# Kernel tuning notes

Hardware: AMD Instinct MI355X
Metric: run time of the kernel (lower is better)

## Reference

```python
import jax, jax.numpy as jnp
import numpy as np

DIM = 384
H = 65536
P = 3
CORR = 2 * 49 * P * P  # 882


def _lin(x, W, b):
    # x: [H, Cin], W: [Cout, Cin], b: [Cout] -> [H, Cout] (1x1 conv == linear over channels)
    return x @ W.T + b


def setup_inputs() -> dict:
    key = jax.random.key(0)
    ks = jax.random.split(key, 20)
    f32 = jnp.float32

    def rn(k, shape, s=0.02):
        return jax.random.normal(k, shape, f32) * s

    return {
        "net": jax.random.normal(ks[0], (1, DIM, H, 1), f32),
        "inp": jax.random.normal(ks[1], (1, DIM, H, 1), f32),
        "corr": jax.random.normal(ks[2], (1, CORR, H, 1), f32),
        "ii": jax.random.normal(ks[3], (1, 1, H, 1), f32),
        "jj": jax.random.normal(ks[4], (1, 1, H, 1), f32),
        "kk": jax.random.normal(ks[5], (1, 1, H, 1), f32),
        # keep_conv: Conv2d(1,1,1,bias=False) with weight zeroed (frozen)
        "kw": jnp.zeros((), f32),
        # corr_conv: Linear(882->384), ReLU, Linear(384->384), ReLU, Linear(384->384)
        "cc_w1": rn(ks[6], (DIM, CORR)), "cc_b1": jnp.zeros((DIM,), f32),
        "cc_w2": rn(ks[7], (DIM, DIM)), "cc_b2": jnp.zeros((DIM,), f32),
        "cc_w3": rn(ks[8], (DIM, DIM)), "cc_b3": jnp.zeros((DIM,), f32),
        # c1 / c2: Linear(384->384), ReLU, Linear(384->384)
        "c1_w1": rn(ks[9], (DIM, DIM)), "c1_b1": jnp.zeros((DIM,), f32),
        "c1_w2": rn(ks[10], (DIM, DIM)), "c1_b2": jnp.zeros((DIM,), f32),
        "c2_w1": rn(ks[11], (DIM, DIM)), "c2_b1": jnp.zeros((DIM,), f32),
        "c2_w2": rn(ks[12], (DIM, DIM)), "c2_b2": jnp.zeros((DIM,), f32),
        # heads: Linear(384->2)
        "d_w": rn(ks[13], (2, DIM)), "d_b": jnp.zeros((2,), f32),
        "w_w": rn(ks[14], (2, DIM)), "w_b": jnp.zeros((2,), f32),
    }


def reference(net, inp, corr, ii, jj, kk, kw,
              cc_w1, cc_b1, cc_w2, cc_b2, cc_w3, cc_b3,
              c1_w1, c1_b1, c1_w2, c1_b2,
              c2_w1, c2_b1, c2_w2, c2_b2,
              d_w, d_b, w_w, w_b):
    # [1,C,H,1] -> [H,C]
    x = net[0, :, :, 0].T
    y = inp[0, :, :, 0].T
    c = corr[0, :, :, 0].T

    # dummy keep_conv path (zero weight, further scaled by 0.0)
    dummy = (ii + jj + kk)[0, 0, :, 0] * kw  # [H]
    x = x + dummy[:, None] * 0.0

    # corr_conv
    cc = _lin(jax.nn.relu(_lin(jax.nn.relu(_lin(c, cc_w1, cc_b1)), cc_w2, cc_b2)), cc_w3, cc_b3)
    x = x + y + cc

    # net = net + c1(net) + c2(net), both branches read the same pre-update net
    b1 = _lin(jax.nn.relu(_lin(x, c1_w1, c1_b1)), c1_w2, c1_b2)
    b2 = _lin(jax.nn.relu(_lin(x, c2_w1, c2_b1)), c2_w2, c2_b2)
    x = x + b1 + b2

    r = jax.nn.relu(x)
    d_out = _lin(r, d_w, d_b)                      # [H,2]
    w_out = jax.nn.sigmoid(_lin(r, w_w, w_b))      # [H,2]

    # back to [1,C,H,1]
    net_out = x.T[None, :, :, None]
    d_out = d_out.T[None, :, :, None]
    w_out = w_out.T[None, :, :, None]
    return (net_out, d_out, w_out)
```

## Files before the change

kernel.cpp:

```cpp
#include <hip/hip_runtime.h>
#include <hip/hip_bf16.h>

#define H 65536
#define DIMC 384

typedef __bf16 bf16x8 __attribute__((ext_vector_type(8)));
typedef float f32x4 __attribute__((ext_vector_type(4)));

__device__ __forceinline__ unsigned short f2bf(float x) {
    return __builtin_bit_cast(unsigned short, __float2bfloat16(x));
}
__device__ __forceinline__ float bf2f(unsigned short u) {
    return __bfloat162float(__builtin_bit_cast(__hip_bfloat16, u));
}

__global__ __launch_bounds__(256) void wconv_k(
    const float* __restrict__ w1, const float* __restrict__ w2, const float* __restrict__ w3,
    const float* __restrict__ c11, const float* __restrict__ c12,
    const float* __restrict__ c21, const float* __restrict__ c22,
    unsigned short* __restrict__ dst)
{
    int m = blockIdx.y;
    const float* src; unsigned short* d; int K, Kp;
    if (m == 0) { src = w1; d = dst; K = 882; Kp = 896; }
    else {
        switch (m) {
            case 1: src = w2;  break;
            case 2: src = w3;  break;
            case 3: src = c11; break;
            case 4: src = c12; break;
            case 5: src = c21; break;
            default: src = c22; break;
        }
        K = 384; Kp = 384;
        d = dst + 344064 + (m - 1) * 147456;
    }
    int gid = blockIdx.x * 256 + threadIdx.x;
    if (gid < 384 * Kp) {
        int n = gid / Kp;
        int k = gid - n * Kp;
        d[gid] = f2bf(k < K ? src[n * K + k] : 0.f);
    }
}

__global__ __launch_bounds__(256) void corr_tconv(const float* __restrict__ src,
                                                  unsigned short* __restrict__ dst)
{
    __shared__ float tile[64][65];
    int hb = blockIdx.x * 64;
    int kb = blockIdx.y * 64;
    int t = threadIdx.x;
    int col = t & 63, r4 = t >> 6;
    #pragma unroll
    for (int p = 0; p < 16; ++p) {
        int row = p * 4 + r4;
        int k = kb + row;
        tile[row][col] = (k < 882) ? src[(size_t)k * H + hb + col] : 0.f;
    }
    __syncthreads();
    #pragma unroll
    for (int p = 0; p < 16; ++p) {
        int hrow = p * 4 + r4;
        dst[(size_t)(hb + hrow) * 896 + kb + col] = f2bf(tile[col][hrow]);
    }
}

__global__ __launch_bounds__(256) void ni_t(const float* __restrict__ a,
                                            const float* __restrict__ b,
                                            float* __restrict__ dst)
{
    __shared__ float tile[64][65];
    int hb = blockIdx.x * 64;
    int cb = blockIdx.y * 64;
    int t = threadIdx.x;
    int col = t & 63, r4 = t >> 6;
    #pragma unroll
    for (int p = 0; p < 16; ++p) {
        int row = p * 4 + r4;
        size_t g = (size_t)(cb + row) * H + hb + col;
        tile[row][col] = a[g] + b[g];
    }
    __syncthreads();
    #pragma unroll
    for (int p = 0; p < 16; ++p) {
        int hrow = p * 4 + r4;
        dst[(size_t)(hb + hrow) * DIMC + cb + col] = tile[col][hrow];
    }
}

__global__ __launch_bounds__(256) void xout_t(const float* __restrict__ src,
                                              float* __restrict__ dst)
{
    __shared__ float tile[64][65];
    int hb = blockIdx.x * 64;
    int cb = blockIdx.y * 64;
    int t = threadIdx.x;
    int col = t & 63, r4 = t >> 6;
    #pragma unroll
    for (int p = 0; p < 16; ++p) {
        int row = p * 4 + r4;
        tile[row][col] = src[(size_t)(hb + row) * DIMC + cb + col];
    }
    __syncthreads();
    #pragma unroll
    for (int p = 0; p < 16; ++p) {
        int crow = p * 4 + r4;
        dst[(size_t)(cb + crow) * H + hb + col] = tile[col][crow];
    }
}

template<int MODE>
__global__ __launch_bounds__(256) void gemm_k(
    const unsigned short* __restrict__ W,
    const unsigned short* __restrict__ A,
    const float* __restrict__ bias,
    const float* __restrict__ auxf,
    const unsigned short* __restrict__ auxb,
    unsigned short* __restrict__ outb,
    float* __restrict__ outf,
    int Kp)
{
    __shared__ unsigned short Wt[128 * 32];
    __shared__ unsigned short At[128 * 32];
    const int tid  = threadIdx.x;
    const int lane = tid & 63;
    const int wave = tid >> 6;
    const int quad = lane >> 4;
    const int l15  = lane & 15;
    const int h0 = blockIdx.x * 128;
    const int c0 = blockIdx.y * 128;
    const int cw = (wave & 1) * 64;
    const int hw = (wave >> 1) * 64;

    const unsigned short* Wbase = W + (size_t)c0 * Kp;
    const unsigned short* Abase = A + (size_t)h0 * Kp;

    f32x4 acc[4][4];
    #pragma unroll
    for (int i = 0; i < 4; ++i)
        #pragma unroll
        for (int j = 0; j < 4; ++j)
            acc[i][j] = f32x4{0.f, 0.f, 0.f, 0.f};

    const int row_l = tid >> 2;
    const int k8    = (tid & 3) * 8;

    for (int kt = 0; kt < Kp; kt += 32) {
        __syncthreads();
        {
            const unsigned short* g0 = Wbase + (size_t)row_l * Kp + kt + k8;
            const unsigned short* g1 = Wbase + (size_t)(row_l + 64) * Kp + kt + k8;
            char* lb0 = (char*)Wt + (wave * 64) * 16;
            char* lb1 = (char*)Wt + (256 + wave * 64) * 16;
            __builtin_amdgcn_global_load_lds((__attribute__((address_space(1))) void*)(void*)g0,
                                             (__attribute__((address_space(3))) void*)lb0, 16, 0, 0);
            __builtin_amdgcn_global_load_lds((__attribute__((address_space(1))) void*)(void*)g1,
                                             (__attribute__((address_space(3))) void*)lb1, 16, 0, 0);
            const unsigned short* a0 = Abase + (size_t)row_l * Kp + kt + k8;
            const unsigned short* a1 = Abase + (size_t)(row_l + 64) * Kp + kt + k8;
            char* la0 = (char*)At + (wave * 64) * 16;
            char* la1 = (char*)At + (256 + wave * 64) * 16;
            __builtin_amdgcn_global_load_lds((__attribute__((address_space(1))) void*)(void*)a0,
                                             (__attribute__((address_space(3))) void*)la0, 16, 0, 0);
            __builtin_amdgcn_global_load_lds((__attribute__((address_space(1))) void*)(void*)a1,
                                             (__attribute__((address_space(3))) void*)la1, 16, 0, 0);
        }
        __syncthreads();

        uint4 aw[4], bx[4];
        const uint4* Wv = (const uint4*)Wt;
        const uint4* Av = (const uint4*)At;
        #pragma unroll
        for (int ci = 0; ci < 4; ++ci) aw[ci] = Wv[(cw + ci * 16 + l15) * 4 + quad];
        #pragma unroll
        for (int hi = 0; hi < 4; ++hi) bx[hi] = Av[(hw + hi * 16 + l15) * 4 + quad];
        #pragma unroll
        for (int ci = 0; ci < 4; ++ci)
            #pragma unroll
            for (int hi = 0; hi < 4; ++hi)
                acc[ci][hi] = __builtin_amdgcn_mfma_f32_16x16x32_bf16(
                    __builtin_bit_cast(bf16x8, aw[ci]),
                    __builtin_bit_cast(bf16x8, bx[hi]),
                    acc[ci][hi], 0, 0, 0);
    }

    #pragma unroll
    for (int ci = 0; ci < 4; ++ci) {
        const int c = c0 + cw + ci * 16 + quad * 4;
        f32x4 b4 = *(const f32x4*)(bias + c);
        #pragma unroll
        for (int hi = 0; hi < 4; ++hi) {
            const int h = h0 + hw + hi * 16 + l15;
            const size_t base = (size_t)h * DIMC + c;
            f32x4 v = acc[ci][hi] + b4;
            if constexpr (MODE == 1) {
                v += *(const f32x4*)(auxf + base);
            }
            if constexpr (MODE == 3) {
                v += *(const f32x4*)(auxf + base);
                ushort4 u = *(const ushort4*)(auxb + base);
                v[0] += bf2f(u.x); v[1] += bf2f(u.y);
                v[2] += bf2f(u.z); v[3] += bf2f(u.w);
            }
            if constexpr (MODE == 1 || MODE == 3) {
                *(f32x4*)(outf + base) = v;
            }
            f32x4 s = v;
            if constexpr (MODE == 0 || MODE == 3) {
                s[0] = fmaxf(s[0], 0.f); s[1] = fmaxf(s[1], 0.f);
                s[2] = fmaxf(s[2], 0.f); s[3] = fmaxf(s[3], 0.f);
            }
            ushort4 o;
            o.x = f2bf(s[0]); o.y = f2bf(s[1]); o.z = f2bf(s[2]); o.w = f2bf(s[3]);
            *(ushort4*)(outb + base) = o;
        }
    }
}

__global__ __launch_bounds__(256) void heads_k(
    const unsigned short* __restrict__ r,
    const float* __restrict__ dW, const float* __restrict__ dB,
    const float* __restrict__ wW, const float* __restrict__ wB,
    float* __restrict__ out)
{
    __shared__ float wl[1536];
    int tid = threadIdx.x;
    for (int i = tid; i < 1536; i += 256)
        wl[i] = (i < 768) ? dW[i] : wW[i - 768];
    __syncthreads();
    int wave = tid >> 6, lane = tid & 63;
    int h = blockIdx.x * 4 + wave;
    const unsigned short* rp = r + (size_t)h * 384 + lane * 6;
    int c = lane * 6;
    float s0 = 0.f, s1 = 0.f, s2 = 0.f, s3 = 0.f;
    #pragma unroll
    for (int i = 0; i < 6; ++i) {
        float rv = bf2f(rp[i]);
        s0 += rv * wl[c + i];
        s1 += rv * wl[384 + c + i];
        s2 += rv * wl[768 + c + i];
        s3 += rv * wl[1152 + c + i];
    }
    #pragma unroll
    for (int m = 32; m >= 1; m >>= 1) {
        s0 += __shfl_xor(s0, m, 64);
        s1 += __shfl_xor(s1, m, 64);
        s2 += __shfl_xor(s2, m, 64);
        s3 += __shfl_xor(s3, m, 64);
    }
    if (lane == 0) {
        float* od = out + (size_t)384 * H;
        float* ow = out + (size_t)386 * H;
        od[h]     = s0 + dB[0];
        od[H + h] = s1 + dB[1];
        ow[h]     = 1.f / (1.f + __expf(-(s2 + wB[0])));
        ow[H + h] = 1.f / (1.f + __expf(-(s3 + wB[1])));
    }
}

extern "C" void kernel_launch(void* const* d_in, const int* in_sizes, int n_in,
                              void* d_out, int out_size, void* d_ws, size_t ws_size,
                              hipStream_t stream)
{
    const float* net   = (const float*)d_in[0];
    const float* inp   = (const float*)d_in[1];
    const float* corr  = (const float*)d_in[2];
    const float* cc_w1 = (const float*)d_in[7];
    const float* cc_b1 = (const float*)d_in[8];
    const float* cc_w2 = (const float*)d_in[9];
    const float* cc_b2 = (const float*)d_in[10];
    const float* cc_w3 = (const float*)d_in[11];
    const float* cc_b3 = (const float*)d_in[12];
    const float* c1_w1 = (const float*)d_in[13];
    const float* c1_b1 = (const float*)d_in[14];
    const float* c1_w2 = (const float*)d_in[15];
    const float* c1_b2 = (const float*)d_in[16];
    const float* c2_w1 = (const float*)d_in[17];
    const float* c2_b1 = (const float*)d_in[18];
    const float* c2_w2 = (const float*)d_in[19];
    const float* c2_b2 = (const float*)d_in[20];
    const float* d_wp  = (const float*)d_in[21];
    const float* d_bp  = (const float*)d_in[22];
    const float* w_wp  = (const float*)d_in[23];
    const float* w_bp  = (const float*)d_in[24];
    float* out = (float*)d_out;

    char* ws = (char*)d_ws;
    size_t off = 0;
    auto carve = [&](size_t bytes) -> char* {
        char* p = ws + off;
        off += (bytes + 255) & ~(size_t)255;
        return p;
    };
    unsigned short* Wreg  = (unsigned short*)carve((size_t)1228800 * 2);
    unsigned short* corrb = (unsigned short*)carve((size_t)H * 896 * 2);
    float*          nib   = (float*)carve((size_t)H * 384 * 4);
    unsigned short* t1    = (unsigned short*)carve((size_t)H * 384 * 2);
    unsigned short* t2    = (unsigned short*)carve((size_t)H * 384 * 2);
    float*          xf    = (float*)carve((size_t)H * 384 * 4);
    unsigned short* xb    = (unsigned short*)carve((size_t)H * 384 * 2);

    unsigned short* w1b  = Wreg;
    unsigned short* w2b  = Wreg + 344064;
    unsigned short* w3b  = w2b + 147456;
    unsigned short* c11b = w3b + 147456;
    unsigned short* c12b = c11b + 147456;
    unsigned short* c21b = c12b + 147456;
    unsigned short* c22b = c21b + 147456;

    wconv_k<<<dim3(1344, 7), 256, 0, stream>>>(cc_w1, cc_w2, cc_w3, c1_w1, c1_w2, c2_w1, c2_w2, Wreg);
    corr_tconv<<<dim3(1024, 14), 256, 0, stream>>>(corr, corrb);
    ni_t<<<dim3(1024, 6), 256, 0, stream>>>(net, inp, nib);

    gemm_k<0><<<dim3(512, 3), 256, 0, stream>>>(w1b, corrb, cc_b1, nullptr, nullptr, t1, nullptr, 896);
    gemm_k<0><<<dim3(512, 3), 256, 0, stream>>>(w2b, t1, cc_b2, nullptr, nullptr, t2, nullptr, 384);
    gemm_k<1><<<dim3(512, 3), 256, 0, stream>>>(w3b, t2, cc_b3, nib, nullptr, xb, xf, 384);
    gemm_k<0><<<dim3(512, 3), 256, 0, stream>>>(c11b, xb, c1_b1, nullptr, nullptr, t1, nullptr, 384);
    gemm_k<2><<<dim3(512, 3), 256, 0, stream>>>(c12b, t1, c1_b2, nullptr, nullptr, t2, nullptr, 384);
    gemm_k<0><<<dim3(512, 3), 256, 0, stream>>>(c21b, xb, c2_b1, nullptr, nullptr, corrb, nullptr, 384);
    gemm_k<3><<<dim3(512, 3), 256, 0, stream>>>(c22b, corrb, c2_b2, xf, t2, t1, nib, 384);

    xout_t<<<dim3(1024, 6), 256, 0, stream>>>(nib, out);
    heads_k<<<H / 4, 256, 0, stream>>>(t1, d_wp, d_bp, w_wp, w_bp, out);
}
```

Before: 1.092 ms.

## Fuse net+inp transpose and output transpose into GEMM epilogues, widen K tile

Drops the separate ni_t and xout_t transpose kernels. The third corr_conv GEMM now reads net and inp directly in channel-major layout in its epilogue, and the last c2 GEMM writes the final net output straight into channel-major layout. The GEMM K-tile also grows from 32 to 64, which halves the barrier and loop iterations at the cost of more LDS. The fused epilogue accesses are strided across lanes (per-channel H-stride reads and writes), so they may coalesce poorly compared with the tiled transposes they replace.

After: 1.014 ms. 7.1% less time.

```diff
diff --git a/kernel.cpp b/kernel.cpp
--- a/kernel.cpp
+++ b/kernel.cpp
@@ -65,63 +65,20 @@
     }
 }
 
-__global__ __launch_bounds__(256) void ni_t(const float* __restrict__ a,
-                                            const float* __restrict__ b,
-                                            float* __restrict__ dst)
-{
-    __shared__ float tile[64][65];
-    int hb = blockIdx.x * 64;
-    int cb = blockIdx.y * 64;
-    int t = threadIdx.x;
-    int col = t & 63, r4 = t >> 6;
-    #pragma unroll
-    for (int p = 0; p < 16; ++p) {
-        int row = p * 4 + r4;
-        size_t g = (size_t)(cb + row) * H + hb + col;
-        tile[row][col] = a[g] + b[g];
-    }
-    __syncthreads();
-    #pragma unroll
-    for (int p = 0; p < 16; ++p) {
-        int hrow = p * 4 + r4;
-        dst[(size_t)(hb + hrow) * DIMC + cb + col] = tile[col][hrow];
-    }
-}
-
-__global__ __launch_bounds__(256) void xout_t(const float* __restrict__ src,
-                                              float* __restrict__ dst)
-{
-    __shared__ float tile[64][65];
-    int hb = blockIdx.x * 64;
-    int cb = blockIdx.y * 64;
-    int t = threadIdx.x;
-    int col = t & 63, r4 = t >> 6;
-    #pragma unroll
-    for (int p = 0; p < 16; ++p) {
-        int row = p * 4 + r4;
-        tile[row][col] = src[(size_t)(hb + row) * DIMC + cb + col];
-    }
-    __syncthreads();
-    #pragma unroll
-    for (int p = 0; p < 16; ++p) {
-        int crow = p * 4 + r4;
-        dst[(size_t)(cb + crow) * H + hb + col] = tile[col][crow];
-    }
-}
-
 template<int MODE>
 __global__ __launch_bounds__(256) void gemm_k(
     const unsigned short* __restrict__ W,
     const unsigned short* __restrict__ A,
     const float* __restrict__ bias,
-    const float* __restrict__ auxf,
+    const float* __restrict__ aux0,
+    const float* __restrict__ aux1,
     const unsigned short* __restrict__ auxb,
     unsigned short* __restrict__ outb,
     float* __restrict__ outf,
     int Kp)
 {
-    __shared__ unsigned short Wt[128 * 32];
-    __shared__ unsigned short At[128 * 32];
+    __shared__ unsigned short Wt[128 * 64];
+    __shared__ unsigned short At[128 * 64];
     const int tid  = threadIdx.x;
     const int lane = tid & 63;
     const int wave = tid >> 6;
@@ -142,46 +99,45 @@
         for (int j = 0; j < 4; ++j)
             acc[i][j] = f32x4{0.f, 0.f, 0.f, 0.f};
 
-    const int row_l = tid >> 2;
-    const int k8    = (tid & 3) * 8;
-
-    for (int kt = 0; kt < Kp; kt += 32) {
+    const int srow = tid >> 3;
+    const int skc  = (tid & 7) * 8;
+
+    for (int kt = 0; kt < Kp; kt += 64) {
         __syncthreads();
-        {
-            const unsigned short* g0 = Wbase + (size_t)row_l * Kp + kt + k8;
-            const unsigned short* g1 = Wbase + (size_t)(row_l + 64) * Kp + kt + k8;
-            char* lb0 = (char*)Wt + (wave * 64) * 16;
-            char* lb1 = (char*)Wt + (256 + wave * 64) * 16;
-            __builtin_amdgcn_global_load_lds((__attribute__((address_space(1))) void*)(void*)g0,
-                                             (__attribute__((address_space(3))) void*)lb0, 16, 0, 0);
-            __builtin_amdgcn_global_load_lds((__attribute__((address_space(1))) void*)(void*)g1,
-                                             (__attribute__((address_space(3))) void*)lb1, 16, 0, 0);
-            const unsigned short* a0 = Abase + (size_t)row_l * Kp + kt + k8;
-            const unsigned short* a1 = Abase + (size_t)(row_l + 64) * Kp + kt + k8;
-            char* la0 = (char*)At + (wave * 64) * 16;
-            char* la1 = (char*)At + (256 + wave * 64) * 16;
-            __builtin_amdgcn_global_load_lds((__attribute__((address_space(1))) void*)(void*)a0,
-                                             (__attribute__((address_space(3))) void*)la0, 16, 0, 0);
-            __builtin_amdgcn_global_load_lds((__attribute__((address_space(1))) void*)(void*)a1,
-                                             (__attribute__((address_space(3))) void*)la1, 16, 0, 0);
+        #pragma unroll
+        for (int i = 0; i < 4; ++i) {
+            const unsigned short* g = Wbase + (size_t)(i * 32 + srow) * Kp + kt + skc;
+            char* lb = (char*)Wt + (i * 256 + wave * 64) * 16;
+            __builtin_amdgcn_global_load_lds((__attribute__((address_space(1))) void*)(void*)g,
+                                             (__attribute__((address_space(3))) void*)lb, 16, 0, 0);
+        }
+        #pragma unroll
+        for (int i = 0; i < 4; ++i) {
+            const unsigned short* g = Abase + (size_t)(i * 32 + srow) * Kp + kt + skc;
+            char* lb = (char*)At + (i * 256 + wave * 64) * 16;
+            __builtin_amdgcn_global_load_lds((__attribute__((address_space(1))) void*)(void*)g,
+                                             (__attribute__((address_space(3))) void*)lb, 16, 0, 0);
         }
         __syncthreads();
 
-        uint4 aw[4], bx[4];
         const uint4* Wv = (const uint4*)Wt;
         const uint4* Av = (const uint4*)At;
         #pragma unroll
-        for (int ci = 0; ci < 4; ++ci) aw[ci] = Wv[(cw + ci * 16 + l15) * 4 + quad];
-        #pragma unroll
-        for (int hi = 0; hi < 4; ++hi) bx[hi] = Av[(hw + hi * 16 + l15) * 4 + quad];
-        #pragma unroll
-        for (int ci = 0; ci < 4; ++ci)
+        for (int ks = 0; ks < 2; ++ks) {
+            uint4 aw[4], bx[4];
             #pragma unroll
-            for (int hi = 0; hi < 4; ++hi)
-                acc[ci][hi] = __builtin_amdgcn_mfma_f32_16x16x32_bf16(
-                    __builtin_bit_cast(bf16x8, aw[ci]),
-                    __builtin_bit_cast(bf16x8, bx[hi]),
-                    acc[ci][hi], 0, 0, 0);
+            for (int ci = 0; ci < 4; ++ci) aw[ci] = Wv[(cw + ci * 16 + l15) * 8 + ks * 4 + quad];
+            #pragma unroll
+            for (int hi = 0; hi < 4; ++hi) bx[hi] = Av[(hw + hi * 16 + l15) * 8 + ks * 4 + quad];
+            #pragma unroll
+            for (int ci = 0; ci < 4; ++ci)
+                #pragma unroll
+                for (int hi = 0; hi < 4; ++hi)
+                    acc[ci][hi] = __builtin_amdgcn_mfma_f32_16x16x32_bf16(
+                        __builtin_bit_cast(bf16x8, aw[ci]),
+                        __builtin_bit_cast(bf16x8, bx[hi]),
+                        acc[ci][hi], 0, 0, 0);
+        }
     }
 
     #pragma unroll
@@ -194,16 +150,23 @@
             const size_t base = (size_t)h * DIMC + c;
             f32x4 v = acc[ci][hi] + b4;
             if constexpr (MODE == 1) {
-                v += *(const f32x4*)(auxf + base);
+                #pragma unroll
+                for (int r = 0; r < 4; ++r)
+                    v[r] += aux0[(size_t)(c + r) * H + h] + aux1[(size_t)(c + r) * H + h];
             }
             if constexpr (MODE == 3) {
-                v += *(const f32x4*)(auxf + base);
+                v += *(const f32x4*)(aux0 + base);
                 ushort4 u = *(const ushort4*)(auxb + base);
                 v[0] += bf2f(u.x); v[1] += bf2f(u.y);
                 v[2] += bf2f(u.z); v[3] += bf2f(u.w);
             }
-            if constexpr (MODE == 1 || MODE == 3) {
+            if constexpr (MODE == 1) {
                 *(f32x4*)(outf + base) = v;
+            }
+            if constexpr (MODE == 3) {
+                #pragma unroll
+                for (int r = 0; r < 4; ++r)
+                    outf[(size_t)(c + r) * H + h] = v[r];
             }
             f32x4 s = v;
             if constexpr (MODE == 0 || MODE == 3) {
@@ -294,7 +257,6 @@
     };
     unsigned short* Wreg  = (unsigned short*)carve((size_t)1228800 * 2);
     unsigned short* corrb = (unsigned short*)carve((size_t)H * 896 * 2);
-    float*          nib   = (float*)carve((size_t)H * 384 * 4);
     unsigned short* t1    = (unsigned short*)carve((size_t)H * 384 * 2);
     unsigned short* t2    = (unsigned short*)carve((size_t)H * 384 * 2);
     float*          xf    = (float*)carve((size_t)H * 384 * 4);
@@ -310,16 +272,14 @@
 
     wconv_k<<<dim3(1344, 7), 256, 0, stream>>>(cc_w1, cc_w2, cc_w3, c1_w1, c1_w2, c2_w1, c2_w2, Wreg);
     corr_tconv<<<dim3(1024, 14), 256, 0, stream>>>(corr, corrb);
-    ni_t<<<dim3(1024, 6), 256, 0, stream>>>(net, inp, nib);
-
-    gemm_k<0><<<dim3(512, 3), 256, 0, stream>>>(w1b, corrb, cc_b1, nullptr, nullptr, t1, nullptr, 896);
-    gemm_k<0><<<dim3(512, 3), 256, 0, stream>>>(w2b, t1, cc_b2, nullptr, nullptr, t2, nullptr, 384);
-    gemm_k<1><<<dim3(512, 3), 256, 0, stream>>>(w3b, t2, cc_b3, nib, nullptr, xb, xf, 384);
-    gemm_k<0><<<dim3(512, 3), 256, 0, stream>>>(c11b, xb, c1_b1, nullptr, nullptr, t1, nullptr, 384);
-    gemm_k<2><<<dim3(512, 3), 256, 0, stream>>>(c12b, t1, c1_b2, nullptr, nullptr, t2, nullptr, 384);
-    gemm_k<0><<<dim3(512, 3), 256, 0, stream>>>(c21b, xb, c2_b1, nullptr, nullptr, corrb, nullptr, 384);
-    gemm_k<3><<<dim3(512, 3), 256, 0, stream>>>(c22b, corrb, c2_b2, xf, t2, t1, nib, 384);
-
-    xout_t<<<dim3(1024, 6), 256, 0, stream>>>(nib, out);
+
+    gemm_k<0><<<dim3(512, 3), 256, 0, stream>>>(w1b, corrb, cc_b1, nullptr, nullptr, nullptr, t1, nullptr, 896);
+    gemm_k<0><<<dim3(512, 3), 256, 0, stream>>>(w2b, t1, cc_b2, nullptr, nullptr, nullptr, t2, nullptr, 384);
+    gemm_k<1><<<dim3(512, 3), 256, 0, stream>>>(w3b, t2, cc_b3, net, inp, nullptr, xb, xf, 384);
+    gemm_k<0><<<dim3(512, 3), 256, 0, stream>>>(c11b, xb, c1_b1, nullptr, nullptr, nullptr, t1, nullptr, 384);
+    gemm_k<2><<<dim3(512, 3), 256, 0, stream>>>(c12b, t1, c1_b2, nullptr, nullptr, nullptr, t2, nullptr, 384);
+    gemm_k<0><<<dim3(512, 3), 256, 0, stream>>>(c21b, xb, c2_b1, nullptr, nullptr, nullptr, corrb, nullptr, 384);
+    gemm_k<3><<<dim3(512, 3), 256, 0, stream>>>(c22b, corrb, c2_b2, xf, nullptr, t2, t1, out, 384);
+
     heads_k<<<H / 4, 256, 0, stream>>>(t1, d_wp, d_bp, w_wp, w_bp, out);
 }
```
